# Performance work log

Measured on AMD Instinct MI355X. Metric: run time of the kernel, lower is better.

Reference implementation:

```python
import jax, jax.numpy as jnp
import numpy as np

MIN_K, MAX_K = 1, 4

def setup_inputs() -> dict:
    key = jax.random.key(0)
    ks = jax.random.split(key, 4)
    B, S, D, E = 8, 4096, 1024, 64
    Dq = D // 4
    s = 0.02
    return {
        "hidden_states": jax.random.normal(ks[0], (B, S, D), dtype=jnp.float32),
        "W_router": jax.random.normal(ks[1], (E, D), dtype=jnp.float32) * s,
        "b_router": jnp.zeros((E,), jnp.float32),
        "W_u1": jax.random.normal(ks[2], (Dq, D), dtype=jnp.float32) * s,
        "b_u1": jnp.zeros((Dq,), jnp.float32),
        "W_u2": jax.random.normal(ks[3], (1, Dq), dtype=jnp.float32) * s,
        "b_u2": jnp.zeros((1,), jnp.float32),
    }

def reference(hidden_states, W_router, b_router, W_u1, b_u1, W_u2, b_u2):
    # uncertainty head: Linear -> GELU(exact) -> Linear -> Sigmoid, squeeze(-1)
    h1 = jax.nn.gelu(jnp.einsum('bsd,qd->bsq', hidden_states, W_u1) + b_u1,
                     approximate=False)
    uncertainty = jax.nn.sigmoid(
        (jnp.einsum('bsq,oq->bso', h1, W_u2) + b_u2)[..., 0])  # [B,S]
    k_float = MIN_K + (MAX_K - MIN_K) * uncertainty
    k_values = jnp.clip(jnp.round(k_float), MIN_K, MAX_K).astype(jnp.int32)

    logits = jnp.einsum('bsd,ed->bse', hidden_states, W_router) + b_router
    top_vals, top_idx = jax.lax.top_k(logits, MAX_K)  # [B,S,MAX_K]

    # per-token dynamic k: keep first k slots, pad values with 0, indices with -1
    pos = jnp.arange(MAX_K)
    valid = pos[None, None, :] < k_values[..., None]  # [B,S,MAX_K]
    weights = jnp.where(valid, top_vals, 0.0)
    indices = jnp.where(valid, top_idx, -1)
    weights = jax.nn.softmax(weights, axis=-1)  # note: padded zeros included, as in original
    return weights, indices, k_values
```

## Files before the change

kernel.cpp:

```cpp
#include <hip/hip_runtime.h>
#include <hip/hip_bf16.h>
#include <math.h>

#define DIM 1024
#define NE  64
#define BM  64
#define NT  32
#define HALF_BYTES 16384
#define BU1_BASE   32768
#define LDS_BYTES  65536

typedef __attribute__((ext_vector_type(8))) short short8;
typedef __attribute__((ext_vector_type(4))) float f32x4;

__device__ __forceinline__ void gload16(const void* gptr, void* lptr) {
  __builtin_amdgcn_global_load_lds(
      (const __attribute__((address_space(1))) unsigned int*)(unsigned long long)gptr,
      (__attribute__((address_space(3))) unsigned int*)(unsigned int)(unsigned long long)lptr,
      16, 0, 0);
}

__device__ __forceinline__ void bsplit(float f, unsigned short& h,
                                       unsigned short& m, unsigned short& l) {
  __hip_bfloat16 bh = __float2bfloat16(f);
  float r1 = f - __bfloat162float(bh);
  __hip_bfloat16 bm = __float2bfloat16(r1);
  __hip_bfloat16 bl = __float2bfloat16(r1 - __bfloat162float(bm));
  h = *reinterpret_cast<unsigned short*>(&bh);
  m = *reinterpret_cast<unsigned short*>(&bm);
  l = *reinterpret_cast<unsigned short*>(&bl);
}

__global__ __launch_bounds__(512)
void ur_hyb(const float* __restrict__ hs,
            const float* __restrict__ Wr,
            const float* __restrict__ br,
            const float* __restrict__ Wu1,
            const float* __restrict__ bu1,
            const float* __restrict__ Wu2,
            const float* __restrict__ bu2,
            float* __restrict__ out,
            int M) {
  __shared__ __align__(16) char smem[LDS_BYTES];

  const int tid = threadIdx.x;
  const int m0 = blockIdx.x * BM;
  const int w2 = tid >> 6, l = tid & 63;
  const int g = l >> 4, c = l & 15;
  const int rcol = 8 * w2 + (l & 7);
  const int jb = l >> 3;

  const int t8 = tid >> 3, k8 = tid & 7;
  const int kx = k8 ^ (t8 & 7);
  const char* pA  = (const char*)hs  + (size_t)(m0 + t8) * 4096 + (kx << 4);
  const char* pBr = (const char*)Wr  + (size_t)t8 * 4096 + (kx << 4);
  const char* pBu = (const char*)Wu1 + (size_t)t8 * 4096 + (kx << 4);
  const unsigned wb = (unsigned)(tid & ~63) * 16u;

  const unsigned axk0 = (unsigned)(((2 * g) ^ (c & 7)) << 4);
  const unsigned axk1 = (unsigned)(((2 * g + 1) ^ (c & 7)) << 4);

  float ar[8];
#pragma unroll
  for (int j = 0; j < 8; ++j) ar[j] = 0.f;
  f32x4 am_[4][2];
#pragma unroll
  for (int s = 0; s < 4; ++s)
#pragma unroll
    for (int n = 0; n < 2; ++n) am_[s][n] = (f32x4){0.f, 0.f, 0.f, 0.f};

  gload16(pA, smem + wb);
  gload16(pBr, smem + 8192 + wb);

  unsigned half = 0;
#pragma unroll 1
  for (int t = 0; t < NT; ++t) {
#pragma unroll
    for (int li = 0; li < 4; ++li)
      gload16(pBu + (size_t)li * 262144, smem + (BU1_BASE + li * 8192 + wb));
    const unsigned oh = half ^ HALF_BYTES;
    if (t != NT - 1) { pA += 128; pBr += 128; pBu += 128; }
    gload16(pA, smem + oh + wb);
    gload16(pBr, smem + (oh + 8192 + wb));

    asm volatile("s_waitcnt vmcnt(6)" ::: "memory");
    __builtin_amdgcn_s_barrier();
    __builtin_amdgcn_sched_barrier(0);

    const char* hb = smem + half;
#pragma unroll
    for (int kq = 0; kq < 8; ++kq) {
      const char* ab = hb + jb * 128 + (((unsigned)(kq ^ jb)) << 4);
      const f32x4 bv = *reinterpret_cast<const f32x4*>(
          hb + 8192 + rcol * 128 + (((unsigned)(kq ^ (l & 7))) << 4));
#pragma unroll
      for (int j = 0; j < 8; ++j) {
        const f32x4 av = *reinterpret_cast<const f32x4*>(ab + j * 1024);
        ar[j] = fmaf(av[0], bv[0], ar[j]);
        ar[j] = fmaf(av[1], bv[1], ar[j]);
        ar[j] = fmaf(av[2], bv[2], ar[j]);
        ar[j] = fmaf(av[3], bv[3], ar[j]);
      }
    }

    asm volatile("s_waitcnt vmcnt(2)" ::: "memory");
    __builtin_amdgcn_s_barrier();
    __builtin_amdgcn_sched_barrier(0);

    short8 Bh[2], Bm[2], Bl[2];
#pragma unroll
    for (int n = 0; n < 2; ++n) {
      const char* bp = smem + BU1_BASE + w2 * 4096 + n * 2048 + c * 128;
      const f32x4 u0 = *reinterpret_cast<const f32x4*>(bp + axk0);
      const f32x4 u1v = *reinterpret_cast<const f32x4*>(bp + axk1);
#pragma unroll
      for (int e = 0; e < 4; ++e) {
        unsigned short h, m, lo;
        bsplit(u0[e], h, m, lo);
        Bh[n][e] = (short)h; Bm[n][e] = (short)m; Bl[n][e] = (short)lo;
        bsplit(u1v[e], h, m, lo);
        Bh[n][4 + e] = (short)h; Bm[n][4 + e] = (short)m; Bl[n][4 + e] = (short)lo;
      }
    }
#pragma unroll
    for (int s = 0; s < 4; ++s) {
      const f32x4 v0 = *reinterpret_cast<const f32x4*>(hb + c * 128 + s * 2048 + axk0);
      const f32x4 v1 = *reinterpret_cast<const f32x4*>(hb + c * 128 + s * 2048 + axk1);
      short8 Ah, Am, Al;
#pragma unroll
      for (int e = 0; e < 4; ++e) {
        unsigned short h, m, lo;
        bsplit(v0[e], h, m, lo);
        Ah[e] = (short)h; Am[e] = (short)m; Al[e] = (short)lo;
        bsplit(v1[e], h, m, lo);
        Ah[4 + e] = (short)h; Am[4 + e] = (short)m; Al[4 + e] = (short)lo;
      }
#pragma unroll
      for (int n = 0; n < 2; ++n) {
        am_[s][n] = __builtin_amdgcn_mfma_f32_16x16x32_bf16(Al, Bh[n], am_[s][n], 0, 0, 0);
        am_[s][n] = __builtin_amdgcn_mfma_f32_16x16x32_bf16(Ah, Bl[n], am_[s][n], 0, 0, 0);
        am_[s][n] = __builtin_amdgcn_mfma_f32_16x16x32_bf16(Am, Bm[n], am_[s][n], 0, 0, 0);
        am_[s][n] = __builtin_amdgcn_mfma_f32_16x16x32_bf16(Am, Bh[n], am_[s][n], 0, 0, 0);
        am_[s][n] = __builtin_amdgcn_mfma_f32_16x16x32_bf16(Ah, Bm[n], am_[s][n], 0, 0, 0);
        am_[s][n] = __builtin_amdgcn_mfma_f32_16x16x32_bf16(Ah, Bh[n], am_[s][n], 0, 0, 0);
      }
    }

    __builtin_amdgcn_s_barrier();
    half = oh;
  }
  __syncthreads();

  float* Lg = reinterpret_cast<float*>(smem);
  float* Xp = reinterpret_cast<float*>(smem + 16640);
  float* Xs = reinterpret_cast<float*>(smem + 49920);

  {
    const float bias = br[rcol];
#pragma unroll
    for (int j = 0; j < 8; ++j) Lg[(jb + 8 * j) * 65 + rcol] = ar[j] + bias;
  }

  float xp[4][4];
#pragma unroll
  for (int s = 0; s < 4; ++s)
#pragma unroll
    for (int reg = 0; reg < 4; ++reg) xp[s][reg] = 0.f;
#pragma unroll
  for (int n = 0; n < 2; ++n) {
    const int qd = 32 * w2 + 16 * n + c;
    const float w2f = Wu2[qd];
    const float b1 = bu1[qd];
#pragma unroll
    for (int s = 0; s < 4; ++s)
#pragma unroll
      for (int reg = 0; reg < 4; ++reg) {
        float h = am_[s][n][reg] + b1;
        float ge = 0.5f * h * (1.f + erff(h * 0.70710678118654752440f));
        xp[s][reg] = fmaf(ge, w2f, xp[s][reg]);
      }
  }
#pragma unroll
  for (int s = 0; s < 4; ++s)
#pragma unroll
    for (int reg = 0; reg < 4; ++reg)
      Xp[(w2 * 16 + c) * 65 + 16 * s + 4 * g + reg] = xp[s][reg];
  __syncthreads();

  if (tid < BM) {
    float x = bu2[0];
#pragma unroll
    for (int cc = 0; cc < 128; ++cc) x += Xp[cc * 65 + tid];
    Xs[tid] = x;
  }
  __syncthreads();

  const size_t Moff_i = 4 * (size_t)M;
  const size_t Moff_k = 8 * (size_t)M;

  for (int t = w2; t < BM; t += 8) {
    float cur = Lg[t * 65 + l];
    float topv[4];
    int topi[4];
#pragma unroll
    for (int s = 0; s < 4; ++s) {
      float mv = cur;
      int mi = l;
#pragma unroll
      for (int off = 32; off >= 1; off >>= 1) {
        float ov = __shfl_xor(mv, off, 64);
        int oi = __shfl_xor(mi, off, 64);
        if (ov > mv || (ov == mv && oi < mi)) { mv = ov; mi = oi; }
      }
      topv[s] = mv;
      topi[s] = mi;
      if (l == mi) cur = -INFINITY;
    }
    if (l == 0) {
      const int token = m0 + t;
      float x = Xs[t];
      float u = 1.f / (1.f + expf(-x));
      float kf = fmaf(3.f, u, 1.f);
      int kv = (int)rintf(kf);
      kv = kv < 1 ? 1 : (kv > 4 ? 4 : kv);

      float wv[4];
#pragma unroll
      for (int s = 0; s < 4; ++s) wv[s] = (s < kv) ? topv[s] : 0.f;
      float mx = fmaxf(fmaxf(wv[0], wv[1]), fmaxf(wv[2], wv[3]));
      float e[4], sum = 0.f;
#pragma unroll
      for (int s = 0; s < 4; ++s) { e[s] = expf(wv[s] - mx); sum += e[s]; }
      float inv = 1.f / sum;
#pragma unroll
      for (int s = 0; s < 4; ++s) {
        out[(size_t)token * 4 + s] = e[s] * inv;
        out[Moff_i + (size_t)token * 4 + s] = (s < kv) ? (float)topi[s] : -1.0f;
      }
      out[Moff_k + token] = (float)kv;
    }
  }
}

extern "C" void kernel_launch(void* const* d_in, const int* in_sizes, int n_in,
                              void* d_out, int out_size, void* d_ws, size_t ws_size,
                              hipStream_t stream) {
  (void)n_in; (void)d_ws; (void)ws_size; (void)out_size;
  const float* hs  = (const float*)d_in[0];
  const float* Wr  = (const float*)d_in[1];
  const float* br  = (const float*)d_in[2];
  const float* Wu1 = (const float*)d_in[3];
  const float* bu1 = (const float*)d_in[4];
  const float* Wu2 = (const float*)d_in[5];
  const float* bu2 = (const float*)d_in[6];
  float* out = (float*)d_out;

  const int M = in_sizes[0] / DIM;
  dim3 grid(M / BM);
  dim3 block(512);
  hipLaunchKernelGGL(ur_hyb, grid, block, 0, stream,
                     hs, Wr, br, Wu1, bu1, Wu2, bu2, out, M);
}
```

Measured before the change: 279.9 us.

## Retile router FMA loop to 4x2 register tile and use truncation-based bf16 split

The router logits FP32 FMA loop now gives each thread a 4-row by 2-column register tile instead of 8 rows by 1 column. This raises reuse of each LDS load and cuts LDS read traffic per FMA. The bf16 three-way split now truncates by masking off the low bits instead of rounding through conversion intrinsics, which takes fewer ALU ops. Two extra MFMA cross terms (Al*Bm and Am*Bl) are added to make up for the precision lost to truncation, raising MFMA work per k-step from 6 to 8.

```diff
diff --git a/kernel.cpp b/kernel.cpp
--- a/kernel.cpp
+++ b/kernel.cpp
@@ -20,15 +20,15 @@
       16, 0, 0);
 }
 
-__device__ __forceinline__ void bsplit(float f, unsigned short& h,
+__device__ __forceinline__ void tsplit(float f, unsigned short& h,
                                        unsigned short& m, unsigned short& l) {
-  __hip_bfloat16 bh = __float2bfloat16(f);
-  float r1 = f - __bfloat162float(bh);
-  __hip_bfloat16 bm = __float2bfloat16(r1);
-  __hip_bfloat16 bl = __float2bfloat16(r1 - __bfloat162float(bm));
-  h = *reinterpret_cast<unsigned short*>(&bh);
-  m = *reinterpret_cast<unsigned short*>(&bm);
-  l = *reinterpret_cast<unsigned short*>(&bl);
+  unsigned fb = __float_as_uint(f);
+  h = (unsigned short)(fb >> 16);
+  float r1 = f - __uint_as_float(fb & 0xFFFF0000u);
+  unsigned r1b = __float_as_uint(r1);
+  m = (unsigned short)(r1b >> 16);
+  float r2 = r1 - __uint_as_float(r1b & 0xFFFF0000u);
+  l = (unsigned short)(__float_as_uint(r2) >> 16);
 }
 
 __global__ __launch_bounds__(512)
@@ -47,8 +47,8 @@
   const int m0 = blockIdx.x * BM;
   const int w2 = tid >> 6, l = tid & 63;
   const int g = l >> 4, c = l & 15;
-  const int rcol = 8 * w2 + (l & 7);
-  const int jb = l >> 3;
+  const int tg = tid >> 5;
+  const int rc = tid & 31;
 
   const int t8 = tid >> 3, k8 = tid & 7;
   const int kx = k8 ^ (t8 & 7);
@@ -60,9 +60,9 @@
   const unsigned axk0 = (unsigned)(((2 * g) ^ (c & 7)) << 4);
   const unsigned axk1 = (unsigned)(((2 * g + 1) ^ (c & 7)) << 4);
 
-  float ar[8];
-#pragma unroll
-  for (int j = 0; j < 8; ++j) ar[j] = 0.f;
+  float ar[4][2];
+#pragma unroll
+  for (int j = 0; j < 4; ++j) { ar[j][0] = 0.f; ar[j][1] = 0.f; }
   f32x4 am_[4][2];
 #pragma unroll
   for (int s = 0; s < 4; ++s)
@@ -90,16 +90,25 @@
     const char* hb = smem + half;
 #pragma unroll
     for (int kq = 0; kq < 8; ++kq) {
-      const char* ab = hb + jb * 128 + (((unsigned)(kq ^ jb)) << 4);
-      const f32x4 bv = *reinterpret_cast<const f32x4*>(
-          hb + 8192 + rcol * 128 + (((unsigned)(kq ^ (l & 7))) << 4));
-#pragma unroll
-      for (int j = 0; j < 8; ++j) {
-        const f32x4 av = *reinterpret_cast<const f32x4*>(ab + j * 1024);
-        ar[j] = fmaf(av[0], bv[0], ar[j]);
-        ar[j] = fmaf(av[1], bv[1], ar[j]);
-        ar[j] = fmaf(av[2], bv[2], ar[j]);
-        ar[j] = fmaf(av[3], bv[3], ar[j]);
+      f32x4 av[4];
+#pragma unroll
+      for (int j = 0; j < 4; ++j) {
+        const int row = 4 * tg + j;
+        av[j] = *reinterpret_cast<const f32x4*>(
+            hb + row * 128 + (((unsigned)(kq ^ (row & 7))) << 4));
+      }
+#pragma unroll
+      for (int n = 0; n < 2; ++n) {
+        const int col = rc + 32 * n;
+        const f32x4 bv = *reinterpret_cast<const f32x4*>(
+            hb + 8192 + col * 128 + (((unsigned)(kq ^ (rc & 7))) << 4));
+#pragma unroll
+        for (int j = 0; j < 4; ++j) {
+          ar[j][n] = fmaf(av[j][0], bv[0], ar[j][n]);
+          ar[j][n] = fmaf(av[j][1], bv[1], ar[j][n]);
+          ar[j][n] = fmaf(av[j][2], bv[2], ar[j][n]);
+          ar[j][n] = fmaf(av[j][3], bv[3], ar[j][n]);
+        }
       }
     }
 
@@ -116,9 +125,9 @@
 #pragma unroll
       for (int e = 0; e < 4; ++e) {
         unsigned short h, m, lo;
-        bsplit(u0[e], h, m, lo);
+        tsplit(u0[e], h, m, lo);
         Bh[n][e] = (short)h; Bm[n][e] = (short)m; Bl[n][e] = (short)lo;
-        bsplit(u1v[e], h, m, lo);
+        tsplit(u1v[e], h, m, lo);
         Bh[n][4 + e] = (short)h; Bm[n][4 + e] = (short)m; Bl[n][4 + e] = (short)lo;
       }
     }
@@ -130,13 +139,15 @@
 #pragma unroll
       for (int e = 0; e < 4; ++e) {
         unsigned short h, m, lo;
-        bsplit(v0[e], h, m, lo);
+        tsplit(v0[e], h, m, lo);
         Ah[e] = (short)h; Am[e] = (short)m; Al[e] = (short)lo;
-        bsplit(v1[e], h, m, lo);
+        tsplit(v1[e], h, m, lo);
         Ah[4 + e] = (short)h; Am[4 + e] = (short)m; Al[4 + e] = (short)lo;
       }
 #pragma unroll
       for (int n = 0; n < 2; ++n) {
+        am_[s][n] = __builtin_amdgcn_mfma_f32_16x16x32_bf16(Al, Bm[n], am_[s][n], 0, 0, 0);
+        am_[s][n] = __builtin_amdgcn_mfma_f32_16x16x32_bf16(Am, Bl[n], am_[s][n], 0, 0, 0);
         am_[s][n] = __builtin_amdgcn_mfma_f32_16x16x32_bf16(Al, Bh[n], am_[s][n], 0, 0, 0);
         am_[s][n] = __builtin_amdgcn_mfma_f32_16x16x32_bf16(Ah, Bl[n], am_[s][n], 0, 0, 0);
         am_[s][n] = __builtin_amdgcn_mfma_f32_16x16x32_bf16(Am, Bm[n], am_[s][n], 0, 0, 0);
@@ -155,10 +166,12 @@
   float* Xp = reinterpret_cast<float*>(smem + 16640);
   float* Xs = reinterpret_cast<float*>(smem + 49920);
 
-  {
-    const float bias = br[rcol];
-#pragma unroll
-    for (int j = 0; j < 8; ++j) Lg[(jb + 8 * j) * 65 + rcol] = ar[j] + bias;
+#pragma unroll
+  for (int n = 0; n < 2; ++n) {
+    const int col = rc + 32 * n;
+    const float bias = br[col];
+#pragma unroll
+    for (int j = 0; j < 4; ++j) Lg[(4 * tg + j) * 65 + col] = ar[j][n] + bias;
   }
 
   float xp[4][4];
```

Measured after the change: 269.5 us. 3.7% less time.
